# Kernel tuning notes

Measured on AMD Instinct MI355X. Metric: run time of the kernel, lower is better.

The kernel has to match this reference:

```python
import jax, jax.numpy as jnp
import numpy as np

NEG_BIG = -9e15
ALPHA = 0.2  # LeakyReLU negative slope


def setup_inputs() -> dict:
    key = jax.random.key(0)
    k1, k2, k3, k4 = jax.random.split(key, 4)
    N, F_in, F_out = 8192, 256, 64
    inp = jax.random.normal(k1, (N, F_in), dtype=jnp.float32)
    adj = jax.random.randint(k2, (N, N), 0, 2, dtype=jnp.int32)
    W = jax.random.normal(k3, (F_in, F_out), dtype=jnp.float32) * 0.05
    a = jax.random.normal(k4, (2 * F_out, 1), dtype=jnp.float32) * 0.05
    return {"input": inp, "adj": adj, "W": W, "a": a}


def reference(input, adj, W, a):
    # h = X W : [N, F_out]
    h = input @ W
    F_out = W.shape[1]
    # a_input[i,j] = concat(h_i, h_j); a_input @ a = h@a1 broadcast over j + h@a2 broadcast over i.
    a1 = a[:F_out, 0]   # [F_out]
    a2 = a[F_out:, 0]   # [F_out]
    s1 = h @ a1         # [N]
    s2 = h @ a2         # [N]
    e = jax.nn.leaky_relu(s1[:, None] + s2[None, :], negative_slope=ALPHA)  # [N, N]
    att = jnp.where(adj > 0, e, jnp.float32(NEG_BIG))
    att = jax.nn.softmax(att, axis=1)
    # dropout is identity in eval mode (training=False)
    h_prime = att @ h   # [N, F_out]
    return jax.nn.elu(h_prime)
```

## Files before the change

### kernel.cpp

```cpp
#include <hip/hip_runtime.h>
#include <hip/hip_bf16.h>

typedef __bf16 bf16_t;
typedef __attribute__((ext_vector_type(8))) __bf16 bf16x8;
typedef __attribute__((ext_vector_type(4))) __bf16 bf16x4;
typedef __attribute__((ext_vector_type(4))) float floatx4;
typedef __attribute__((ext_vector_type(4))) int intx4;
typedef __attribute__((ext_vector_type(4))) unsigned uintx4;

#define NN 8192
#define FIN 256
#define FOUT 64
#define GAT_ALPHA 0.2f
#define JSPLIT 4
#define JSEG (NN / JSPLIT)
#define PHASEJ 256
#define NPHASE (JSEG / PHASEJ)
#define ADJ_STRIDE 260

__global__ __launch_bounds__(256) void gat_h_kernel(
    const float* __restrict__ input,
    const float* __restrict__ W,
    const float* __restrict__ a,
    bf16_t* __restrict__ hT,
    float* __restrict__ e1g, float* __restrict__ f1g,
    unsigned* __restrict__ ef2g)
{
    alignas(16) __shared__ bf16_t in_lds[32][264];
    alignas(16) __shared__ bf16_t wt_lds[64][264];
    __shared__ float h_lds[32][65];

    const int t  = threadIdx.x;
    const int i0 = blockIdx.x * 32;

    #pragma unroll
    for (int v = 0; v < 8; v++) {
        int u  = v * 256 + t;
        int i  = u >> 6;
        int k4 = (u & 63) * 4;
        floatx4 x = *(const floatx4*)(input + (size_t)(i0 + i) * FIN + k4);
        bf16x4 b;
        #pragma unroll
        for (int e = 0; e < 4; e++) b[e] = (bf16_t)x[e];
        *(bf16x4*)(&in_lds[i][k4]) = b;
    }
    #pragma unroll
    for (int v = 0; v < 16; v++) {
        int u  = v * 256 + t;
        int k  = u >> 4;
        int f4 = (u & 15) * 4;
        floatx4 wv = *(const floatx4*)(W + k * FOUT + f4);
        #pragma unroll
        for (int e = 0; e < 4; e++) wt_lds[f4 + e][k] = (bf16_t)wv[e];
    }
    __syncthreads();

    const int wave = t >> 6;
    const int lane = t & 63;
    const int i16  = (wave & 1) * 16;
    const int f32  = (wave >> 1) * 32;
    const int lm   = lane & 15;
    const int lq   = lane >> 4;

    floatx4 acc0 = {0.f, 0.f, 0.f, 0.f};
    floatx4 acc1 = {0.f, 0.f, 0.f, 0.f};
    #pragma unroll
    for (int ks = 0; ks < 8; ks++) {
        int ko = ks * 32 + lq * 8;
        bf16x8 af = *(const bf16x8*)(&in_lds[i16 + lm][ko]);
        bf16x8 b0 = *(const bf16x8*)(&wt_lds[f32 + lm][ko]);
        bf16x8 b1 = *(const bf16x8*)(&wt_lds[f32 + 16 + lm][ko]);
        acc0 = __builtin_amdgcn_mfma_f32_16x16x32_bf16(af, b0, acc0, 0, 0, 0);
        acc1 = __builtin_amdgcn_mfma_f32_16x16x32_bf16(af, b1, acc1, 0, 0, 0);
    }

    #pragma unroll
    for (int c = 0; c < 2; c++) {
        floatx4 acc = c ? acc1 : acc0;
        int f  = f32 + c * 16 + lm;
        int ib = i0 + i16 + lq * 4;
        bf16x4 hp;
        #pragma unroll
        for (int r = 0; r < 4; r++) hp[r] = (bf16_t)acc[r];
        *(bf16x4*)(hT + (size_t)f * NN + ib) = hp;
    }
    #pragma unroll
    for (int c = 0; c < 2; c++) {
        floatx4 acc = c ? acc1 : acc0;
        #pragma unroll
        for (int r = 0; r < 4; r++)
            h_lds[i16 + lq * 4 + r][f32 + c * 16 + lm] = acc[r];
    }
    __syncthreads();

    if (t < 64) {
        int r   = t & 31;
        int sel = t >> 5;
        const float* av = a + sel * FOUT;
        float s = 0.f;
        #pragma unroll 8
        for (int f = 0; f < FOUT; f++) s += h_lds[r][f] * av[f];
        int gi = i0 + r;
        float E = expf(s);
        float F = expf(GAT_ALPHA * s);
        if (sel == 0) {
            e1g[gi] = E; f1g[gi] = F;
        } else {
            unsigned eb = __builtin_bit_cast(unsigned short, (bf16_t)E);
            unsigned fb = __builtin_bit_cast(unsigned short, (bf16_t)F);
            ef2g[gi] = (fb << 16) | eb;
        }
    }
}

__global__ __launch_bounds__(128, 2) void gat_att_kernel(
    const int* __restrict__ adj,
    const bf16_t* __restrict__ hT,
    const float* __restrict__ e1g, const float* __restrict__ f1g,
    const unsigned* __restrict__ ef2g,
    float* __restrict__ pacc,
    float* __restrict__ prs)
{
    __shared__ int alds[2][16 * ADJ_STRIDE];

    const int t    = threadIdx.x;
    const int wave = t >> 6;
    const int lane = t & 63;
    const int m    = lane & 15;
    const int q    = lane >> 4;
    const int i0   = blockIdx.x * 32 + wave * 16;
    const int js   = blockIdx.y;
    const int jb   = js * JSEG;
    const int row  = i0 + m;

    int* lds = alds[wave];

    const float E1 = e1g[row];
    const float F1 = f1g[row];

    floatx4 acc[4];
    #pragma unroll
    for (int c = 0; c < 4; c++) acc[c] = (floatx4){0.f, 0.f, 0.f, 0.f};
    float rowsum = 0.f;

    intx4 g[16];
    #pragma unroll
    for (int r = 0; r < 16; r++)
        g[r] = *(const intx4*)(adj + (size_t)(i0 + r) * NN + jb + 4 * lane);

    for (int p = 0; p < NPHASE; p++) {
        __builtin_amdgcn_s_waitcnt(0xC07F);

        #pragma unroll
        for (int r = 0; r < 16; r++)
            *(intx4*)(lds + r * ADJ_STRIDE + 4 * lane) = g[r];

        if (p + 1 < NPHASE) {
            #pragma unroll
            for (int r = 0; r < 16; r++)
                g[r] = *(const intx4*)(adj + (size_t)(i0 + r) * NN + jb
                                       + (p + 1) * PHASEJ + 4 * lane);
        }

        const unsigned* efp = ef2g + jb + p * PHASEJ + q * 8;
        const bf16_t*   htp = hT + (size_t)m * NN + jb + p * PHASEJ + q * 8;
        const int*      ap  = lds + m * ADJ_STRIDE + q * 8;

        uintx4 e0 = *(const uintx4*)(efp);
        uintx4 e1 = *(const uintx4*)(efp + 4);
        bf16x8 hb[4];
        #pragma unroll
        for (int c = 0; c < 4; c++)
            hb[c] = *(const bf16x8*)(htp + (size_t)c * 16 * NN);

        #pragma unroll
        for (int ks = 0; ks < 8; ks++) {
            intx4 a0 = *(const intx4*)(ap + ks * 32);
            intx4 a1 = *(const intx4*)(ap + ks * 32 + 4);

            uintx4 ce0 = e0, ce1 = e1;
            bf16x8 chb0 = hb[0], chb1 = hb[1], chb2 = hb[2], chb3 = hb[3];
            if (ks < 7) {
                e0 = *(const uintx4*)(efp + (ks + 1) * 32);
                e1 = *(const uintx4*)(efp + (ks + 1) * 32 + 4);
                #pragma unroll
                for (int c = 0; c < 4; c++)
                    hb[c] = *(const bf16x8*)(htp + (size_t)c * 16 * NN
                                             + (ks + 1) * 32);
            }

            bf16x8 wf;
            #pragma unroll
            for (int e = 0; e < 8; e++) {
                int av     = (e < 4) ? a0[e] : a1[e - 4];
                unsigned v = (e < 4) ? ce0[e] : ce1[e - 4];
                float e2 = __builtin_bit_cast(float, v << 16);
                float f2 = __builtin_bit_cast(float, v & 0xffff0000u);
                float pv = fmaxf(E1 * e2, F1 * f2);
                float wv = (av > 0) ? pv : 0.f;
                bf16_t wb = (bf16_t)wv;
                wf[e] = wb;
                rowsum += (float)wb;
            }
            acc[0] = __builtin_amdgcn_mfma_f32_16x16x32_bf16(wf, chb0, acc[0], 0, 0, 0);
            acc[1] = __builtin_amdgcn_mfma_f32_16x16x32_bf16(wf, chb1, acc[1], 0, 0, 0);
            acc[2] = __builtin_amdgcn_mfma_f32_16x16x32_bf16(wf, chb2, acc[2], 0, 0, 0);
            acc[3] = __builtin_amdgcn_mfma_f32_16x16x32_bf16(wf, chb3, acc[3], 0, 0, 0);
        }
    }

    rowsum += __shfl_xor(rowsum, 16, 64);
    rowsum += __shfl_xor(rowsum, 32, 64);
    if (lane < 16) prs[(size_t)js * NN + i0 + lane] = rowsum;

    float* pa = pacc + (size_t)js * NN * FOUT;
    #pragma unroll
    for (int c = 0; c < 4; c++) {
        #pragma unroll
        for (int r = 0; r < 4; r++)
            pa[(size_t)(i0 + q * 4 + r) * FOUT + c * 16 + m] = acc[c][r];
    }
}

__global__ __launch_bounds__(256) void gat_combine_kernel(
    const float* __restrict__ pacc,
    const float* __restrict__ prs,
    float* __restrict__ out)
{
    int idx = blockIdx.x * 256 + threadIdx.x;
    int i   = idx >> 4;
    floatx4 s = {0.f, 0.f, 0.f, 0.f};
    float rs  = 0.f;
    #pragma unroll
    for (int js = 0; js < JSPLIT; js++) {
        s  += *(const floatx4*)(pacc + (size_t)js * NN * FOUT + (size_t)idx * 4);
        rs += prs[(size_t)js * NN + i];
    }
    float rinv = (rs > 0.f) ? 1.0f / rs : 0.f;
    floatx4 r;
    #pragma unroll
    for (int e = 0; e < 4; e++) {
        float x = s[e] * rinv;
        r[e] = (x > 0.f) ? x : (expf(x) - 1.0f);
    }
    *(floatx4*)(out + (size_t)idx * 4) = r;
}

extern "C" void kernel_launch(void* const* d_in, const int* in_sizes, int n_in,
                              void* d_out, int out_size, void* d_ws, size_t ws_size,
                              hipStream_t stream) {
    const float* input = (const float*)d_in[0];
    const int*   adj   = (const int*)d_in[1];
    const float* W     = (const float*)d_in[2];
    const float* a     = (const float*)d_in[3];
    float*       out   = (float*)d_out;

    char* ws = (char*)d_ws;
    bf16_t*   hT   = (bf16_t*)ws;
    float*    e1g  = (float*)(ws + (1 << 20));
    float*    f1g  = e1g + NN;
    unsigned* ef2g = (unsigned*)(f1g + NN);
    float*    pacc = (float*)(ef2g + NN);
    float*    prs  = pacc + (size_t)JSPLIT * NN * FOUT;

    gat_h_kernel<<<NN / 32, 256, 0, stream>>>(input, W, a, hT, e1g, f1g, ef2g);

    dim3 gridB(NN / 32, JSPLIT);
    gat_att_kernel<<<gridB, 128, 0, stream>>>(adj, hT, e1g, f1g, ef2g,
                                              pacc, prs);

    gat_combine_kernel<<<NN * FOUT / 4 / 256, 256, 0, stream>>>(pacc, prs, out);
}
```

Baseline: 400.4 us.

## Add producer wave streaming adjacency into LDS via direct global-to-LDS loads

Adds a third wave per block that loads adjacency tiles straight into double-buffered shared memory with global_load_lds, with barriers handing each phase to the two compute waves. Those waves no longer stage adjacency through registers, and their ef2g/hT prefetch now runs across phase boundaries. The per-row sum also moves from scalar adds into an extra MFMA against a ones vector. The aim is to overlap the adjacency stream with compute and cut VGPR pressure, at the cost of one extra MFMA per step and block-wide barrier synchronisation.

```diff
diff --git a/kernel.cpp b/kernel.cpp
--- a/kernel.cpp
+++ b/kernel.cpp
@@ -16,7 +16,8 @@
 #define JSEG (NN / JSPLIT)
 #define PHASEJ 256
 #define NPHASE (JSEG / PHASEJ)
-#define ADJ_STRIDE 260
+#define NSTEPS (JSEG / 32)
+#define ROWSTRIDE 268
 
 __global__ __launch_bounds__(256) void gat_h_kernel(
     const float* __restrict__ input,
@@ -113,7 +114,7 @@
     }
 }
 
-__global__ __launch_bounds__(128, 2) void gat_att_kernel(
+__global__ __launch_bounds__(192) void gat_att_kernel(
     const int* __restrict__ adj,
     const bf16_t* __restrict__ hT,
     const float* __restrict__ e1g, const float* __restrict__ f1g,
@@ -121,57 +122,74 @@
     float* __restrict__ pacc,
     float* __restrict__ prs)
 {
-    __shared__ int alds[2][16 * ADJ_STRIDE];
+    __shared__ int abuf[2][32 * ROWSTRIDE];
 
     const int t    = threadIdx.x;
     const int wave = t >> 6;
     const int lane = t & 63;
-    const int m    = lane & 15;
-    const int q    = lane >> 4;
-    const int i0   = blockIdx.x * 32 + wave * 16;
+    const int bx   = blockIdx.x;
     const int js   = blockIdx.y;
     const int jb   = js * JSEG;
-    const int row  = i0 + m;
-
-    int* lds = alds[wave];
-
-    const float E1 = e1g[row];
-    const float F1 = f1g[row];
+    const int bi0  = bx * 32;
+
+    if (wave == 2) {
+        #pragma unroll
+        for (int r = 0; r < 32; r++)
+            __builtin_amdgcn_global_load_lds(
+                (const __attribute__((address_space(1))) unsigned*)
+                    (adj + (size_t)(bi0 + r) * NN + jb + lane * 4),
+                (__attribute__((address_space(3))) unsigned*)
+                    (&abuf[0][r * ROWSTRIDE]),
+                16, 0, 0);
+        for (int p = 0; p < NPHASE; p++) {
+            asm volatile("s_waitcnt vmcnt(0)" ::: "memory");
+            asm volatile("s_barrier" ::: "memory");
+            if (p + 1 < NPHASE) {
+                int* dst = abuf[(p + 1) & 1];
+                #pragma unroll
+                for (int r = 0; r < 32; r++)
+                    __builtin_amdgcn_global_load_lds(
+                        (const __attribute__((address_space(1))) unsigned*)
+                            (adj + (size_t)(bi0 + r) * NN + jb
+                             + (p + 1) * PHASEJ + lane * 4),
+                        (__attribute__((address_space(3))) unsigned*)
+                            (dst + r * ROWSTRIDE),
+                        16, 0, 0);
+            }
+        }
+        return;
+    }
+
+    const int m   = lane & 15;
+    const int q   = lane >> 4;
+    const int i0  = bi0 + wave * 16;
+    const int lr  = wave * 16 + m;
+
+    const float E1 = e1g[i0 + m];
+    const float F1 = f1g[i0 + m];
+
+    const unsigned* efp = ef2g + jb + q * 8;
+    const bf16_t*   htp = hT + (size_t)m * NN + jb + q * 8;
 
     floatx4 acc[4];
     #pragma unroll
     for (int c = 0; c < 4; c++) acc[c] = (floatx4){0.f, 0.f, 0.f, 0.f};
-    float rowsum = 0.f;
-
-    intx4 g[16];
-    #pragma unroll
-    for (int r = 0; r < 16; r++)
-        g[r] = *(const intx4*)(adj + (size_t)(i0 + r) * NN + jb + 4 * lane);
+    floatx4 acc4 = {0.f, 0.f, 0.f, 0.f};
+
+    bf16x8 ones8;
+    #pragma unroll
+    for (int e = 0; e < 8; e++) ones8[e] = (bf16_t)1.0f;
+
+    uintx4 e0 = *(const uintx4*)(efp);
+    uintx4 e1 = *(const uintx4*)(efp + 4);
+    bf16x8 hb[4];
+    #pragma unroll
+    for (int c = 0; c < 4; c++)
+        hb[c] = *(const bf16x8*)(htp + (size_t)c * 16 * NN);
 
     for (int p = 0; p < NPHASE; p++) {
-        __builtin_amdgcn_s_waitcnt(0xC07F);
-
-        #pragma unroll
-        for (int r = 0; r < 16; r++)
-            *(intx4*)(lds + r * ADJ_STRIDE + 4 * lane) = g[r];
-
-        if (p + 1 < NPHASE) {
-            #pragma unroll
-            for (int r = 0; r < 16; r++)
-                g[r] = *(const intx4*)(adj + (size_t)(i0 + r) * NN + jb
-                                       + (p + 1) * PHASEJ + 4 * lane);
-        }
-
-        const unsigned* efp = ef2g + jb + p * PHASEJ + q * 8;
-        const bf16_t*   htp = hT + (size_t)m * NN + jb + p * PHASEJ + q * 8;
-        const int*      ap  = lds + m * ADJ_STRIDE + q * 8;
-
-        uintx4 e0 = *(const uintx4*)(efp);
-        uintx4 e1 = *(const uintx4*)(efp + 4);
-        bf16x8 hb[4];
-        #pragma unroll
-        for (int c = 0; c < 4; c++)
-            hb[c] = *(const bf16x8*)(htp + (size_t)c * 16 * NN);
+        asm volatile("s_barrier" ::: "memory");
+        const int* ap = abuf[p & 1] + lr * ROWSTRIDE + q * 8;
 
         #pragma unroll
         for (int ks = 0; ks < 8; ks++) {
@@ -179,14 +197,15 @@
             intx4 a1 = *(const intx4*)(ap + ks * 32 + 4);
 
             uintx4 ce0 = e0, ce1 = e1;
-            bf16x8 chb0 = hb[0], chb1 = hb[1], chb2 = hb[2], chb3 = hb[3];
-            if (ks < 7) {
-                e0 = *(const uintx4*)(efp + (ks + 1) * 32);
-                e1 = *(const uintx4*)(efp + (ks + 1) * 32 + 4);
+            bf16x8 ch0 = hb[0], ch1 = hb[1], ch2 = hb[2], ch3 = hb[3];
+            const int s = p * 8 + ks;
+            if (s + 1 < NSTEPS) {
+                e0 = *(const uintx4*)(efp + (s + 1) * 32);
+                e1 = *(const uintx4*)(efp + (s + 1) * 32 + 4);
                 #pragma unroll
                 for (int c = 0; c < 4; c++)
                     hb[c] = *(const bf16x8*)(htp + (size_t)c * 16 * NN
-                                             + (ks + 1) * 32);
+                                             + (s + 1) * 32);
             }
 
             bf16x8 wf;
@@ -197,21 +216,21 @@
                 float e2 = __builtin_bit_cast(float, v << 16);
                 float f2 = __builtin_bit_cast(float, v & 0xffff0000u);
                 float pv = fmaxf(E1 * e2, F1 * f2);
-                float wv = (av > 0) ? pv : 0.f;
-                bf16_t wb = (bf16_t)wv;
-                wf[e] = wb;
-                rowsum += (float)wb;
+                wf[e] = (bf16_t)((av > 0) ? pv : 0.f);
             }
-            acc[0] = __builtin_amdgcn_mfma_f32_16x16x32_bf16(wf, chb0, acc[0], 0, 0, 0);
-            acc[1] = __builtin_amdgcn_mfma_f32_16x16x32_bf16(wf, chb1, acc[1], 0, 0, 0);
-            acc[2] = __builtin_amdgcn_mfma_f32_16x16x32_bf16(wf, chb2, acc[2], 0, 0, 0);
-            acc[3] = __builtin_amdgcn_mfma_f32_16x16x32_bf16(wf, chb3, acc[3], 0, 0, 0);
+            acc[0] = __builtin_amdgcn_mfma_f32_16x16x32_bf16(wf, ch0, acc[0], 0, 0, 0);
+            acc[1] = __builtin_amdgcn_mfma_f32_16x16x32_bf16(wf, ch1, acc[1], 0, 0, 0);
+            acc[2] = __builtin_amdgcn_mfma_f32_16x16x32_bf16(wf, ch2, acc[2], 0, 0, 0);
+            acc[3] = __builtin_amdgcn_mfma_f32_16x16x32_bf16(wf, ch3, acc[3], 0, 0, 0);
+            acc4   = __builtin_amdgcn_mfma_f32_16x16x32_bf16(wf, ones8, acc4, 0, 0, 0);
         }
     }
 
-    rowsum += __shfl_xor(rowsum, 16, 64);
-    rowsum += __shfl_xor(rowsum, 32, 64);
-    if (lane < 16) prs[(size_t)js * NN + i0 + lane] = rowsum;
+    if (m == 0) {
+        #pragma unroll
+        for (int r = 0; r < 4; r++)
+            prs[(size_t)js * NN + i0 + q * 4 + r] = acc4[r];
+    }
 
     float* pa = pacc + (size_t)js * NN * FOUT;
     #pragma unroll
@@ -266,7 +285,7 @@
     gat_h_kernel<<<NN / 32, 256, 0, stream>>>(input, W, a, hT, e1g, f1g, ef2g);
 
     dim3 gridB(NN / 32, JSPLIT);
-    gat_att_kernel<<<gridB, 128, 0, stream>>>(adj, hT, e1g, f1g, ef2g,
+    gat_att_kernel<<<gridB, 192, 0, stream>>>(adj, hT, e1g, f1g, ef2g,
                                               pacc, prs);
 
     gat_combine_kernel<<<NN * FOUT / 4 / 256, 256, 0, stream>>>(pacc, prs, out);
```

After: 434.0 us. 8.4% more time.
